# Kernel tuning notes

Hardware: AMD Instinct MI355X
Metric: run time of the kernel (lower is better)

Reference implementation:

```python
import jax, jax.numpy as jnp
import numpy as np

TAU = 2.0        # leak time constant
CLAMP = 1000.0   # state clamp in LeakyRNN.recurrence
EPS = 1e-4       # eps in PolicyRNN.evaluate

B, T, H, NI, NA = 64, 2048, 256, 4, 2


def setup_inputs() -> dict:
    key = jax.random.key(0)
    ks = jax.random.split(key, 10)
    state = jax.random.normal(ks[0], (B, T, NI), jnp.float32)
    last_action = jax.random.normal(ks[1], (B, T, NA), jnp.float32)
    reward = jax.random.randint(ks[2], (B, T, NA), 0, 2).astype(jnp.float32)
    hidden_in = jnp.zeros((B, H), jnp.float32)
    W1 = jax.random.normal(ks[3], (H, NI + 2 * NA), jnp.float32) * np.float32(np.sqrt(2.0 / (NI + 2 * NA)))
    b1 = jnp.zeros((H,), jnp.float32)
    Wih = jax.random.normal(ks[4], (H, H), jnp.float32) * np.float32(np.sqrt(2.0 / H))
    Whh_raw = jax.random.normal(ks[5], (H, H), jnp.float32) * np.float32(0.5 / np.sqrt(H))
    W2 = jax.random.normal(ks[6], (H, H), jnp.float32) * np.float32(np.sqrt(2.0 / H))
    b2 = jnp.zeros((H,), jnp.float32)
    W3 = jax.random.normal(ks[7], (NA, H), jnp.float32) * np.float32(np.sqrt(2.0 / H))
    b3 = jnp.zeros((NA,), jnp.float32)
    Qs = jax.random.normal(ks[8], (B, T, NA), jnp.float32)
    # MultLayerAdaptiveSimple with alphas=[1,0]: weight1=[1,0], weight2=[0,1]
    mix_w = jnp.array([[1.0, 0.0], [0.0, 1.0]], jnp.float32)
    return dict(state=state, last_action=last_action, reward=reward,
                hidden_in=hidden_in, W1=W1, b1=b1, Wih=Wih, Whh_raw=Whh_raw,
                W2=W2, b2=b2, W3=W3, b3=b3, Qs=Qs, mix_w=mix_w)


def reference(state, last_action, reward, hidden_in, W1, b1, Wih, Whh_raw,
              W2, b2, W3, b3, Qs, mix_w):
    # (B,T,.) -> (T,B,.) time-major, matching permute(1,0,2)
    x = jnp.concatenate([reward, state, last_action], -1).transpose(1, 0, 2)
    x = jax.nn.relu(x @ W1.T + b1)                     # linear1 + relu

    # IdentityDiagonal parametrization: zero diagonal, subtract I/tau
    Whh = Whh_raw - jnp.diag(jnp.diag(Whh_raw)) - jnp.eye(H, dtype=Whh_raw.dtype) / TAU
    u = x @ Wih.T                                      # precompute input drive (T,B,H)
    leak = 1.0 - 1.0 / TAU

    def step(h, ut):
        h_new = jnp.clip(leak * h + ut + jax.nn.relu(h) @ Whh.T, -CLAMP, CLAMP)
        return h_new, h_new

    hidden_out, ys = jax.lax.scan(step, hidden_in, u)  # ys: (T,B,H)

    y = jax.nn.relu(ys @ W2.T + b2) @ W3.T + b3        # linear2+relu, linear3
    probs = y.transpose(1, 0, 2)                       # (B,T,NA)

    # evaluate() deterministic path with reward-indexed adaptive mixing
    z = (probs == 0.0).astype(probs.dtype) * EPS
    logp = jnp.log(jax.nn.softmax(probs, -1) + z)
    logq = jnp.log(jax.nn.softmax(Qs, -1) + z)
    # SumOne parametrization (p=1) on each MultLayer 2-vector
    w = jnp.clip(mix_w, -1.0, 1.0)
    table = w / jnp.sum(jnp.abs(w), axis=1, keepdims=True)   # (2,2)
    sel = table[reward[:, :, 0].astype(jnp.int32)]           # (B,T,2)
    mixed = logp * sel[..., :1] + logq * sel[..., 1:2]
    return jnp.exp(mixed), hidden_out
```

## Files before the change

### kernel.cpp

```cpp
#include <hip/hip_runtime.h>
#include <hip/hip_bf16.h>
#include <math.h>

#define Bn 64
#define Tn 2048
#define Hn 256

constexpr float LEAK    = 0.5f;
constexpr float NEGDIAG = -0.5f;
constexpr float CLAMP_V = 1000.0f;
constexpr float EPS_V   = 1e-4f;

typedef __attribute__((ext_vector_type(8))) short  short8;
typedef __attribute__((ext_vector_type(4))) float  f32x4;

#define FAST_BARRIER() do {                                   \
    asm volatile("s_waitcnt lgkmcnt(0)" ::: "memory");        \
    __builtin_amdgcn_s_barrier();                             \
    asm volatile("" ::: "memory");                            \
  } while (0)

__device__ inline short bf16_rne(float x) {
  __hip_bfloat16 h = __float2bfloat16(x);
  return *reinterpret_cast<short*>(&h);
}
__device__ inline float bf16_to_f(short s) {
  union { unsigned u; float f; } c; c.u = ((unsigned)(unsigned short)s) << 16;
  return c.f;
}
__device__ inline unsigned pack2(short a, short b) {
  return (unsigned)(unsigned short)a | ((unsigned)(unsigned short)b << 16);
}

#define SA 40

__global__ __launch_bounds__(512) void g_u(
    const float* __restrict__ reward, const float* __restrict__ state,
    const float* __restrict__ last_action, const float* __restrict__ W1,
    const float* __restrict__ b1, const float* __restrict__ Wih,
    float* __restrict__ u)
{
  __shared__ short Ah[128*SA], Al[128*SA], Bh[256*SA], Bl[256*SA];
  __shared__ __align__(16) float inp_s[128][8];
  __shared__ __align__(16) float w1_s[256][8];
  __shared__ float b1_s[256];
  const int tid = threadIdx.x;
  const int r0  = blockIdx.x * 128;

  for (int idx = tid; idx < 2048; idx += 512) ((float*)w1_s)[idx] = W1[idx];
  if (tid < 256) b1_s[tid] = b1[tid];
  for (int idx = tid; idx < 1024; idx += 512) {
    int rr = idx >> 3, i = idx & 7;
    int r = r0 + rr, b = r & 63, t = r >> 6;
    long base = (long)b * Tn + t;
    float v;
    if (i < 2)      v = reward[base * 2 + i];
    else if (i < 6) v = state[base * 4 + (i - 2)];
    else            v = last_action[base * 2 + (i - 6)];
    inp_s[rr][i] = v;
  }

  const int w    = tid >> 6, lane = tid & 63;
  const int wm   = w >> 2, wn = w & 3;
  const int fr   = lane & 15, fk = lane >> 4;
  f32x4 acc[4][4];
  #pragma unroll
  for (int a = 0; a < 4; ++a)
    #pragma unroll
    for (int c = 0; c < 4; ++c) acc[a][c] = (f32x4){0.f, 0.f, 0.f, 0.f};

  __syncthreads();

  for (int ks = 0; ks < 8; ++ks) {
    const int k0 = ks * 32;
    if (ks) __syncthreads();
    for (int p = tid; p < 2048; p += 512) {
      int rr = p >> 4, kp = (p & 15) * 2;
      int k = k0 + kp;
      float4 iv0 = *reinterpret_cast<const float4*>(&inp_s[rr][0]);
      float4 iv1 = *reinterpret_cast<const float4*>(&inp_s[rr][4]);
      float4 wa0 = *reinterpret_cast<const float4*>(&w1_s[k][0]);
      float4 wa1 = *reinterpret_cast<const float4*>(&w1_s[k][4]);
      float4 wb0 = *reinterpret_cast<const float4*>(&w1_s[k+1][0]);
      float4 wb1 = *reinterpret_cast<const float4*>(&w1_s[k+1][4]);
      float s0 = b1_s[k], s1 = b1_s[k+1];
      s0 = fmaf(iv0.x, wa0.x, s0); s0 = fmaf(iv0.y, wa0.y, s0);
      s0 = fmaf(iv0.z, wa0.z, s0); s0 = fmaf(iv0.w, wa0.w, s0);
      s0 = fmaf(iv1.x, wa1.x, s0); s0 = fmaf(iv1.y, wa1.y, s0);
      s0 = fmaf(iv1.z, wa1.z, s0); s0 = fmaf(iv1.w, wa1.w, s0);
      s1 = fmaf(iv0.x, wb0.x, s1); s1 = fmaf(iv0.y, wb0.y, s1);
      s1 = fmaf(iv0.z, wb0.z, s1); s1 = fmaf(iv0.w, wb0.w, s1);
      s1 = fmaf(iv1.x, wb1.x, s1); s1 = fmaf(iv1.y, wb1.y, s1);
      s1 = fmaf(iv1.z, wb1.z, s1); s1 = fmaf(iv1.w, wb1.w, s1);
      float v0 = fmaxf(s0, 0.f), v1 = fmaxf(s1, 0.f);
      short h0 = bf16_rne(v0), h1 = bf16_rne(v1);
      short l0 = bf16_rne(v0 - bf16_to_f(h0)), l1 = bf16_rne(v1 - bf16_to_f(h1));
      int off = rr * SA + kp;
      *reinterpret_cast<unsigned*>(&Ah[off]) = pack2(h0, h1);
      *reinterpret_cast<unsigned*>(&Al[off]) = pack2(l0, l1);
    }
    for (int c = tid; c < 2048; c += 512) {
      int n = c >> 3, kc = (c & 7) * 4;
      float4 f = *reinterpret_cast<const float4*>(&Wih[n * 256 + k0 + kc]);
      short h0 = bf16_rne(f.x), h1 = bf16_rne(f.y), h2 = bf16_rne(f.z), h3 = bf16_rne(f.w);
      short l0 = bf16_rne(f.x - bf16_to_f(h0)), l1 = bf16_rne(f.y - bf16_to_f(h1));
      short l2 = bf16_rne(f.z - bf16_to_f(h2)), l3 = bf16_rne(f.w - bf16_to_f(h3));
      int off = n * SA + kc;
      *reinterpret_cast<uint2*>(&Bh[off]) = make_uint2(pack2(h0, h1), pack2(h2, h3));
      *reinterpret_cast<uint2*>(&Bl[off]) = make_uint2(pack2(l0, l1), pack2(l2, l3));
    }
    __syncthreads();
    short8 bhf[4], blf[4];
    #pragma unroll
    for (int nf = 0; nf < 4; ++nf) {
      const int brow = wn * 64 + nf * 16 + fr;
      bhf[nf] = *reinterpret_cast<const short8*>(&Bh[brow * SA + fk * 8]);
      blf[nf] = *reinterpret_cast<const short8*>(&Bl[brow * SA + fk * 8]);
    }
    #pragma unroll
    for (int mf = 0; mf < 4; ++mf) {
      const int arow = wm * 64 + mf * 16 + fr;
      short8 ah = *reinterpret_cast<const short8*>(&Ah[arow * SA + fk * 8]);
      short8 al = *reinterpret_cast<const short8*>(&Al[arow * SA + fk * 8]);
      #pragma unroll
      for (int nf = 0; nf < 4; ++nf) {
        acc[mf][nf] = __builtin_amdgcn_mfma_f32_16x16x32_bf16(ah, bhf[nf], acc[mf][nf], 0, 0, 0);
        acc[mf][nf] = __builtin_amdgcn_mfma_f32_16x16x32_bf16(ah, blf[nf], acc[mf][nf], 0, 0, 0);
        acc[mf][nf] = __builtin_amdgcn_mfma_f32_16x16x32_bf16(al, bhf[nf], acc[mf][nf], 0, 0, 0);
      }
    }
  }
  #pragma unroll
  for (int mf = 0; mf < 4; ++mf) {
    const int rbase = r0 + wm * 64 + mf * 16 + (lane >> 4) * 4;
    #pragma unroll
    for (int nf = 0; nf < 4; ++nf) {
      const int n = wn * 64 + nf * 16 + fr;
      #pragma unroll
      for (int j = 0; j < 4; ++j)
        u[(long)(rbase + j) * Hn + n] = acc[mf][nf][j];
    }
  }
}

__global__ __launch_bounds__(1024, 4) void k_scan(
    const float* __restrict__ Whh_raw, const float* __restrict__ hidden_in,
    float* __restrict__ ubuf, float* __restrict__ out)
{
  __shared__ __align__(16) float rh[2][256];
  const int tid = threadIdx.x;
  const int w = tid >> 6;
  const int l = tid & 63;
  const int g = l & 15;
  const int o = l >> 4;
  const int b = blockIdx.x;
  const int kbase = g << 4;

  float wgt[4][16];
  #pragma unroll
  for (int m = 0; m < 4; ++m) {
    const int j = (w << 4) + (o << 2) + m;
    #pragma unroll
    for (int i = 0; i < 16; ++i) {
      const int k = kbase + i;
      float v = Whh_raw[j * 256 + k];
      wgt[m][i] = (k == j) ? NEGDIAG : v;
    }
  }

  const int b0 = g & 1, b1 = (g >> 1) & 1;
  const bool owner = (g < 4);
  const int m_own = (b0 << 1) | b1;
  const int j_own = (w << 4) + (o << 2) + m_own;

  const int wr_off = (j_own & ~15) | ((((j_own >> 2) + (j_own >> 5)) & 3) << 2)
                   | (j_own & 3);

  float h = 0.f, u_cur = 0.f;
  if (owner) {
    h     = hidden_in[b * Hn + j_own];
    u_cur = ubuf[b * Hn + j_own];
  }
  const float* u_ptr  = ubuf + ((long)Bn + b) * Hn + j_own;
  float*       ys_ptr = ubuf + (long)b * Hn + j_own;

  #pragma unroll 2
  for (int t = 0; t < Tn; ++t) {
    const int p = t & 1;
    if (owner) rh[p][wr_off] = fmaxf(h, 0.f);
    FAST_BARRIER();

    float u_nxt = 0.f;
    if (owner && t < Tn - 1) u_nxt = *u_ptr;

    float v0 = 0.f, v1 = 0.f, v2 = 0.f, v3 = 0.f;
    const float* base = &rh[p][kbase];
    #pragma unroll
    for (int q = 0; q < 4; ++q) {
      const int rot = ((((g >> 1) + q) & 3) << 2);
      const float4 r4 = *reinterpret_cast<const float4*>(base + rot);
      v0 = fmaf(r4.x, wgt[0][4*q+0], v0);
      v0 = fmaf(r4.y, wgt[0][4*q+1], v0);
      v0 = fmaf(r4.z, wgt[0][4*q+2], v0);
      v0 = fmaf(r4.w, wgt[0][4*q+3], v0);
      v1 = fmaf(r4.x, wgt[1][4*q+0], v1);
      v1 = fmaf(r4.y, wgt[1][4*q+1], v1);
      v1 = fmaf(r4.z, wgt[1][4*q+2], v1);
      v1 = fmaf(r4.w, wgt[1][4*q+3], v1);
      v2 = fmaf(r4.x, wgt[2][4*q+0], v2);
      v2 = fmaf(r4.y, wgt[2][4*q+1], v2);
      v2 = fmaf(r4.z, wgt[2][4*q+2], v2);
      v2 = fmaf(r4.w, wgt[2][4*q+3], v2);
      v3 = fmaf(r4.x, wgt[3][4*q+0], v3);
      v3 = fmaf(r4.y, wgt[3][4*q+1], v3);
      v3 = fmaf(r4.z, wgt[3][4*q+2], v3);
      v3 = fmaf(r4.w, wgt[3][4*q+3], v3);
    }

    const float s00 = b0 ? v0 : v2;
    const float k00 = b0 ? v2 : v0;
    const float s01 = b0 ? v1 : v3;
    const float k01 = b0 ? v3 : v1;
    const float t00 = k00 + __shfl_xor(s00, 1);
    const float t01 = k01 + __shfl_xor(s01, 1);
    const float s1 = b1 ? t00 : t01;
    const float k1 = b1 ? t01 : t00;
    float s = k1 + __shfl_xor(s1, 2);
    s += __shfl_xor(s, 4);
    s += __shfl_xor(s, 8);

    if (owner) {
      float hn = fmaf(LEAK, h, u_cur) + s;
      hn = fminf(fmaxf(hn, -CLAMP_V), CLAMP_V);
      *ys_ptr = hn;
      h = hn; u_cur = u_nxt;
    }
    ys_ptr += Bn * Hn;
    u_ptr  += Bn * Hn;
  }
  if (owner) out[(long)Bn * Tn * 2 + b * Hn + j_own] = h;
}

__global__ __launch_bounds__(512) void g_out(
    const float* __restrict__ ys, const float* __restrict__ W2,
    const float* __restrict__ b2, const float* __restrict__ W3,
    float* __restrict__ yout)
{
  __shared__ short Ah[128*SA], Al[128*SA], Bh[256*SA], Bl[256*SA];
  __shared__ float b2_s[256];
  __shared__ float w3_s[512];
  const int tid = threadIdx.x;
  const int r0  = blockIdx.x * 128;

  if (tid < 256) b2_s[tid] = b2[tid];
  if (tid < 512) w3_s[tid] = W3[tid];

  const int w    = tid >> 6, lane = tid & 63;
  const int wm   = w >> 2, wn = w & 3;
  const int fr   = lane & 15, fk = lane >> 4;
  f32x4 acc[4][4];
  #pragma unroll
  for (int a = 0; a < 4; ++a)
    #pragma unroll
    for (int c = 0; c < 4; ++c) acc[a][c] = (f32x4){0.f, 0.f, 0.f, 0.f};

  __syncthreads();

  for (int ks = 0; ks < 8; ++ks) {
    const int k0 = ks * 32;
    if (ks) __syncthreads();
    for (int c = tid; c < 1024; c += 512) {
      int rr = c >> 3, kc = (c & 7) * 4;
      float4 f = *reinterpret_cast<const float4*>(&ys[(long)(r0 + rr) * Hn + k0 + kc]);
      short h0 = bf16_rne(f.x), h1 = bf16_rne(f.y), h2 = bf16_rne(f.z), h3 = bf16_rne(f.w);
      short l0 = bf16_rne(f.x - bf16_to_f(h0)), l1 = bf16_rne(f.y - bf16_to_f(h1));
      short l2 = bf16_rne(f.z - bf16_to_f(h2)), l3 = bf16_rne(f.w - bf16_to_f(h3));
      int off = rr * SA + kc;
      *reinterpret_cast<uint2*>(&Ah[off]) = make_uint2(pack2(h0, h1), pack2(h2, h3));
      *reinterpret_cast<uint2*>(&Al[off]) = make_uint2(pack2(l0, l1), pack2(l2, l3));
    }
    for (int c = tid; c < 2048; c += 512) {
      int n = c >> 3, kc = (c & 7) * 4;
      float4 f = *reinterpret_cast<const float4*>(&W2[n * 256 + k0 + kc]);
      short h0 = bf16_rne(f.x), h1 = bf16_rne(f.y), h2 = bf16_rne(f.z), h3 = bf16_rne(f.w);
      short l0 = bf16_rne(f.x - bf16_to_f(h0)), l1 = bf16_rne(f.y - bf16_to_f(h1));
      short l2 = bf16_rne(f.z - bf16_to_f(h2)), l3 = bf16_rne(f.w - bf16_to_f(h3));
      int off = n * SA + kc;
      *reinterpret_cast<uint2*>(&Bh[off]) = make_uint2(pack2(h0, h1), pack2(h2, h3));
      *reinterpret_cast<uint2*>(&Bl[off]) = make_uint2(pack2(l0, l1), pack2(l2, l3));
    }
    __syncthreads();
    short8 bhf[4], blf[4];
    #pragma unroll
    for (int nf = 0; nf < 4; ++nf) {
      const int brow = wn * 64 + nf * 16 + fr;
      bhf[nf] = *reinterpret_cast<const short8*>(&Bh[brow * SA + fk * 8]);
      blf[nf] = *reinterpret_cast<const short8*>(&Bl[brow * SA + fk * 8]);
    }
    #pragma unroll
    for (int mf = 0; mf < 4; ++mf) {
      const int arow = wm * 64 + mf * 16 + fr;
      short8 ah = *reinterpret_cast<const short8*>(&Ah[arow * SA + fk * 8]);
      short8 al = *reinterpret_cast<const short8*>(&Al[arow * SA + fk * 8]);
      #pragma unroll
      for (int nf = 0; nf < 4; ++nf) {
        acc[mf][nf] = __builtin_amdgcn_mfma_f32_16x16x32_bf16(ah, bhf[nf], acc[mf][nf], 0, 0, 0);
        acc[mf][nf] = __builtin_amdgcn_mfma_f32_16x16x32_bf16(ah, blf[nf], acc[mf][nf], 0, 0, 0);
        acc[mf][nf] = __builtin_amdgcn_mfma_f32_16x16x32_bf16(al, bhf[nf], acc[mf][nf], 0, 0, 0);
      }
    }
  }

  float yp[4][4][2];
  #pragma unroll
  for (int mf = 0; mf < 4; ++mf)
    #pragma unroll
    for (int j = 0; j < 4; ++j) { yp[mf][j][0] = 0.f; yp[mf][j][1] = 0.f; }

  #pragma unroll
  for (int mf = 0; mf < 4; ++mf)
    #pragma unroll
    for (int nf = 0; nf < 4; ++nf) {
      const int n = wn * 64 + nf * 16 + fr;
      const float b2v = b2_s[n];
      const float w30 = w3_s[n], w31 = w3_s[256 + n];
      #pragma unroll
      for (int j = 0; j < 4; ++j) {
        float v = fmaxf(acc[mf][nf][j] + b2v, 0.f);
        yp[mf][j][0] = fmaf(v, w30, yp[mf][j][0]);
        yp[mf][j][1] = fmaf(v, w31, yp[mf][j][1]);
      }
    }
  #pragma unroll
  for (int off = 1; off < 16; off <<= 1) {
    #pragma unroll
    for (int mf = 0; mf < 4; ++mf)
      #pragma unroll
      for (int j = 0; j < 4; ++j) {
        yp[mf][j][0] += __shfl_xor(yp[mf][j][0], off);
        yp[mf][j][1] += __shfl_xor(yp[mf][j][1], off);
      }
  }

  __syncthreads();
  float* yred = reinterpret_cast<float*>(Ah);
  if (fr == 0) {
    #pragma unroll
    for (int mf = 0; mf < 4; ++mf)
      #pragma unroll
      for (int j = 0; j < 4; ++j) {
        int rl = wm * 64 + mf * 16 + (lane >> 4) * 4 + j;
        yred[(rl * 2 + 0) * 4 + wn] = yp[mf][j][0];
        yred[(rl * 2 + 1) * 4 + wn] = yp[mf][j][1];
      }
  }
  __syncthreads();
  if (tid < 256) {
    int rl = tid >> 1, a = tid & 1;
    const float* yr = &yred[(rl * 2 + a) * 4];
    float y = (yr[0] + yr[1]) + (yr[2] + yr[3]);
    int r = r0 + rl, b = r & 63, t = r >> 6;
    yout[((long)b * Tn + t) * 2 + a] = y;
  }
}

__global__ __launch_bounds__(256) void k_head(
    float* __restrict__ out, const float* __restrict__ Qs,
    const float* __restrict__ reward, const float* __restrict__ mix_w,
    const float* __restrict__ b3)
{
  const int idx = blockIdx.x * 256 + threadIdx.x;
  if (idx >= Bn * Tn) return;
  const long base = (long)idx * 2;
  float y0 = out[base]     + b3[0];
  float y1 = out[base + 1] + b3[1];
  float z0 = (y0 == 0.f) ? EPS_V : 0.f;
  float z1 = (y1 == 0.f) ? EPS_V : 0.f;

  float m  = fmaxf(y0, y1);
  float e0 = expf(y0 - m), e1 = expf(y1 - m), es = e0 + e1;
  float sp0 = e0 / es, sp1 = e1 / es;

  float q0 = Qs[base], q1 = Qs[base + 1];
  float mq = fmaxf(q0, q1);
  float f0 = expf(q0 - mq), f1 = expf(q1 - mq), fs = f0 + f1;
  float sq0 = f0 / fs, sq1 = f1 / fs;

  int ri = (int)reward[base];
  float m0 = fminf(fmaxf(mix_w[ri * 2 + 0], -1.f), 1.f);
  float m1 = fminf(fmaxf(mix_w[ri * 2 + 1], -1.f), 1.f);
  float den = fabsf(m0) + fabsf(m1);
  float s0 = m0 / den, s1 = m1 / den;

  out[base]     = expf(s0 * logf(sp0 + z0) + s1 * logf(sq0 + z0));
  out[base + 1] = expf(s0 * logf(sp1 + z1) + s1 * logf(sq1 + z1));
}

extern "C" void kernel_launch(void* const* d_in, const int* in_sizes, int n_in,
                              void* d_out, int out_size, void* d_ws, size_t ws_size,
                              hipStream_t stream)
{
  const float* state       = (const float*)d_in[0];
  const float* last_action = (const float*)d_in[1];
  const float* reward      = (const float*)d_in[2];
  const float* hidden_in   = (const float*)d_in[3];
  const float* W1          = (const float*)d_in[4];
  const float* b1          = (const float*)d_in[5];
  const float* Wih         = (const float*)d_in[6];
  const float* Whh_raw     = (const float*)d_in[7];
  const float* W2          = (const float*)d_in[8];
  const float* b2          = (const float*)d_in[9];
  const float* W3          = (const float*)d_in[10];
  const float* b3          = (const float*)d_in[11];
  const float* Qs          = (const float*)d_in[12];
  const float* mix_w       = (const float*)d_in[13];
  float* out = (float*)d_out;
  float* u   = (float*)d_ws;

  const int nrows = Tn * Bn;
  g_u   <<<nrows / 128, 512, 0, stream>>>(reward, state, last_action, W1, b1, Wih, u);
  k_scan<<<Bn,          1024, 0, stream>>>(Whh_raw, hidden_in, u, out);
  g_out <<<nrows / 128, 512, 0, stream>>>(u, W2, b2, W3, out);
  k_head<<<nrows / 256, 256, 0, stream>>>(out, Qs, reward, mix_w, b3);
}
```

Measured before the change: 1.700 ms.

## Run recurrent scan matvec on MFMA with split-bf16 weights and state

The per-timestep Whh·relu(h) product moves from scalar FP32 FMAs plus shuffle reductions over a 1024-thread block to bf16 MFMA instructions in a 256-thread block. Weights and relu(h) are each split into hi and lo bf16 parts, and three MFMAs recover near-FP32 accuracy. The h vector is broadcast across all 16 B columns, so most of each MFMA's work is redundant. The aim is to shorten the serial per-step latency and use a cheaper barrier over fewer waves. The cost is slightly lower precision than true FP32 and heavy register use for the split weights.

```diff
diff --git a/kernel.cpp b/kernel.cpp
--- a/kernel.cpp
+++ b/kernel.cpp
@@ -143,102 +143,133 @@
   }
 }
 
-__global__ __launch_bounds__(1024, 4) void k_scan(
+__global__ __launch_bounds__(256) void k_scan(
     const float* __restrict__ Whh_raw, const float* __restrict__ hidden_in,
     float* __restrict__ ubuf, float* __restrict__ out)
 {
-  __shared__ __align__(16) float rh[2][256];
-  const int tid = threadIdx.x;
-  const int w = tid >> 6;
-  const int l = tid & 63;
-  const int g = l & 15;
-  const int o = l >> 4;
-  const int b = blockIdx.x;
-  const int kbase = g << 4;
-
-  float wgt[4][16];
-  #pragma unroll
-  for (int m = 0; m < 4; ++m) {
-    const int j = (w << 4) + (o << 2) + m;
-    #pragma unroll
-    for (int i = 0; i < 16; ++i) {
-      const int k = kbase + i;
-      float v = Whh_raw[j * 256 + k];
-      wgt[m][i] = (k == j) ? NEGDIAG : v;
-    }
-  }
-
-  const int b0 = g & 1, b1 = (g >> 1) & 1;
-  const bool owner = (g < 4);
-  const int m_own = (b0 << 1) | b1;
-  const int j_own = (w << 4) + (o << 2) + m_own;
-
-  const int wr_off = (j_own & ~15) | ((((j_own >> 2) + (j_own >> 5)) & 3) << 2)
-                   | (j_own & 3);
-
-  float h = 0.f, u_cur = 0.f;
+  __shared__ __align__(16) short rh_s[2][2][256];
+  const int tid  = threadIdx.x;
+  const int w    = tid >> 6;
+  const int lane = tid & 63;
+  const int fr   = lane & 15;
+  const int fk   = lane >> 4;
+  const int b    = blockIdx.x;
+  const bool owner = (fr == 0);
+
+  short8 whi[4][8], wlo[4][8];
+  #pragma unroll
+  for (int mt = 0; mt < 4; ++mt) {
+    const int j = (w * 4 + mt) * 16 + fr;
+    #pragma unroll
+    for (int kt = 0; kt < 8; ++kt) {
+      const int kb = kt * 32 + fk * 8;
+      float4 f0 = *reinterpret_cast<const float4*>(&Whh_raw[j * 256 + kb]);
+      float4 f1 = *reinterpret_cast<const float4*>(&Whh_raw[j * 256 + kb + 4]);
+      float v[8] = {f0.x, f0.y, f0.z, f0.w, f1.x, f1.y, f1.z, f1.w};
+      #pragma unroll
+      for (int e = 0; e < 8; ++e) {
+        if (kb + e == j) v[e] = NEGDIAG;
+        short h = bf16_rne(v[e]);
+        whi[mt][kt][e] = h;
+        wlo[mt][kt][e] = bf16_rne(v[e] - bf16_to_f(h));
+      }
+    }
+  }
+
+  const int fq = lane >> 4;
+  const int jb = w * 64 + fq * 4;
+  float4 h4[4], u4[4];
   if (owner) {
-    h     = hidden_in[b * Hn + j_own];
-    u_cur = ubuf[b * Hn + j_own];
-  }
-  const float* u_ptr  = ubuf + ((long)Bn + b) * Hn + j_own;
-  float*       ys_ptr = ubuf + (long)b * Hn + j_own;
+    #pragma unroll
+    for (int mt = 0; mt < 4; ++mt) {
+      h4[mt] = *reinterpret_cast<const float4*>(&hidden_in[b * Hn + jb + mt * 16]);
+      u4[mt] = *reinterpret_cast<const float4*>(&ubuf[(long)b * Hn + jb + mt * 16]);
+    }
+    #pragma unroll
+    for (int mt = 0; mt < 4; ++mt) {
+      const int j0 = jb + mt * 16;
+      short hh[4], ll[4];
+      #pragma unroll
+      for (int e = 0; e < 4; ++e) {
+        float rv = fmaxf(h4[mt][e], 0.f);
+        hh[e] = bf16_rne(rv);
+        ll[e] = bf16_rne(rv - bf16_to_f(hh[e]));
+      }
+      *reinterpret_cast<uint2*>(&rh_s[0][0][j0]) = make_uint2(pack2(hh[0], hh[1]), pack2(hh[2], hh[3]));
+      *reinterpret_cast<uint2*>(&rh_s[0][1][j0]) = make_uint2(pack2(ll[0], ll[1]), pack2(ll[2], ll[3]));
+    }
+  }
+  __syncthreads();
+
+  const float* u_ptr  = ubuf + ((long)Bn + b) * Hn + jb;
+  float*       ys_ptr = ubuf + (long)b * Hn + jb;
 
   #pragma unroll 2
   for (int t = 0; t < Tn; ++t) {
     const int p = t & 1;
-    if (owner) rh[p][wr_off] = fmaxf(h, 0.f);
+    short8 bh[8], bl[8];
+    #pragma unroll
+    for (int kt = 0; kt < 8; ++kt) {
+      bh[kt] = *reinterpret_cast<const short8*>(&rh_s[p][0][kt * 32 + fk * 8]);
+      bl[kt] = *reinterpret_cast<const short8*>(&rh_s[p][1][kt * 32 + fk * 8]);
+    }
+    float4 un[4];
+    if (owner && t < Tn - 1) {
+      #pragma unroll
+      for (int mt = 0; mt < 4; ++mt)
+        un[mt] = *reinterpret_cast<const float4*>(u_ptr + mt * 16);
+    }
+
+    f32x4 a1[4], a2[4], a3[4];
+    #pragma unroll
+    for (int mt = 0; mt < 4; ++mt) {
+      a1[mt] = (f32x4){0.f, 0.f, 0.f, 0.f};
+      a2[mt] = (f32x4){0.f, 0.f, 0.f, 0.f};
+      a3[mt] = (f32x4){0.f, 0.f, 0.f, 0.f};
+    }
+    #pragma unroll
+    for (int kt = 0; kt < 8; ++kt)
+      #pragma unroll
+      for (int mt = 0; mt < 4; ++mt) {
+        a1[mt] = __builtin_amdgcn_mfma_f32_16x16x32_bf16(whi[mt][kt], bh[kt], a1[mt], 0, 0, 0);
+        a2[mt] = __builtin_amdgcn_mfma_f32_16x16x32_bf16(whi[mt][kt], bl[kt], a2[mt], 0, 0, 0);
+        a3[mt] = __builtin_amdgcn_mfma_f32_16x16x32_bf16(wlo[mt][kt], bh[kt], a3[mt], 0, 0, 0);
+      }
+
+    if (owner) {
+      const int p2 = p ^ 1;
+      #pragma unroll
+      for (int mt = 0; mt < 4; ++mt) {
+        const int j0 = jb + mt * 16;
+        float4 hn;
+        short hh[4], ll[4];
+        #pragma unroll
+        for (int e = 0; e < 4; ++e) {
+          float s = (a1[mt][e] + a2[mt][e]) + a3[mt][e];
+          float v = fmaf(LEAK, h4[mt][e], u4[mt][e]) + s;
+          v = fminf(fmaxf(v, -CLAMP_V), CLAMP_V);
+          hn[e] = v;
+          float rv = fmaxf(v, 0.f);
+          hh[e] = bf16_rne(rv);
+          ll[e] = bf16_rne(rv - bf16_to_f(hh[e]));
+        }
+        *reinterpret_cast<float4*>(ys_ptr + mt * 16) = hn;
+        *reinterpret_cast<uint2*>(&rh_s[p2][0][j0]) = make_uint2(pack2(hh[0], hh[1]), pack2(hh[2], hh[3]));
+        *reinterpret_cast<uint2*>(&rh_s[p2][1][j0]) = make_uint2(pack2(ll[0], ll[1]), pack2(ll[2], ll[3]));
+        h4[mt] = hn;
+        u4[mt] = un[mt];
+      }
+    }
     FAST_BARRIER();
-
-    float u_nxt = 0.f;
-    if (owner && t < Tn - 1) u_nxt = *u_ptr;
-
-    float v0 = 0.f, v1 = 0.f, v2 = 0.f, v3 = 0.f;
-    const float* base = &rh[p][kbase];
-    #pragma unroll
-    for (int q = 0; q < 4; ++q) {
-      const int rot = ((((g >> 1) + q) & 3) << 2);
-      const float4 r4 = *reinterpret_cast<const float4*>(base + rot);
-      v0 = fmaf(r4.x, wgt[0][4*q+0], v0);
-      v0 = fmaf(r4.y, wgt[0][4*q+1], v0);
-      v0 = fmaf(r4.z, wgt[0][4*q+2], v0);
-      v0 = fmaf(r4.w, wgt[0][4*q+3], v0);
-      v1 = fmaf(r4.x, wgt[1][4*q+0], v1);
-      v1 = fmaf(r4.y, wgt[1][4*q+1], v1);
-      v1 = fmaf(r4.z, wgt[1][4*q+2], v1);
-      v1 = fmaf(r4.w, wgt[1][4*q+3], v1);
-      v2 = fmaf(r4.x, wgt[2][4*q+0], v2);
-      v2 = fmaf(r4.y, wgt[2][4*q+1], v2);
-      v2 = fmaf(r4.z, wgt[2][4*q+2], v2);
-      v2 = fmaf(r4.w, wgt[2][4*q+3], v2);
-      v3 = fmaf(r4.x, wgt[3][4*q+0], v3);
-      v3 = fmaf(r4.y, wgt[3][4*q+1], v3);
-      v3 = fmaf(r4.z, wgt[3][4*q+2], v3);
-      v3 = fmaf(r4.w, wgt[3][4*q+3], v3);
-    }
-
-    const float s00 = b0 ? v0 : v2;
-    const float k00 = b0 ? v2 : v0;
-    const float s01 = b0 ? v1 : v3;
-    const float k01 = b0 ? v3 : v1;
-    const float t00 = k00 + __shfl_xor(s00, 1);
-    const float t01 = k01 + __shfl_xor(s01, 1);
-    const float s1 = b1 ? t00 : t01;
-    const float k1 = b1 ? t01 : t00;
-    float s = k1 + __shfl_xor(s1, 2);
-    s += __shfl_xor(s, 4);
-    s += __shfl_xor(s, 8);
-
-    if (owner) {
-      float hn = fmaf(LEAK, h, u_cur) + s;
-      hn = fminf(fmaxf(hn, -CLAMP_V), CLAMP_V);
-      *ys_ptr = hn;
-      h = hn; u_cur = u_nxt;
-    }
     ys_ptr += Bn * Hn;
     u_ptr  += Bn * Hn;
   }
-  if (owner) out[(long)Bn * Tn * 2 + b * Hn + j_own] = h;
+
+  if (owner) {
+    #pragma unroll
+    for (int mt = 0; mt < 4; ++mt)
+      *reinterpret_cast<float4*>(&out[(long)Bn * Tn * 2 + b * Hn + jb + mt * 16]) = h4[mt];
+  }
 }
 
 __global__ __launch_bounds__(512) void g_out(
@@ -419,7 +450,7 @@
 
   const int nrows = Tn * Bn;
   g_u   <<<nrows / 128, 512, 0, stream>>>(reward, state, last_action, W1, b1, Wih, u);
-  k_scan<<<Bn,          1024, 0, stream>>>(Whh_raw, hidden_in, u, out);
+  k_scan<<<Bn,           256, 0, stream>>>(Whh_raw, hidden_in, u, out);
   g_out <<<nrows / 128, 512, 0, stream>>>(u, W2, b2, W3, out);
   k_head<<<nrows / 256, 256, 0, stream>>>(out, Qs, reward, mix_w, b3);
 }
```

Result: slower. 3.099 ms (+82.2%).

## Use packed FMA, ds_swizzle reductions, and deeper u prefetch in recurrent scan

Applied to the files above, without the earlier changes.

The per-step matvec in the sequential scan now uses v_pk_fma_f32 on pairs of weights, which halves the FMA instruction count, and keeps two partial accumulators per output. The cross-lane reductions switch from __shfl_xor (ds_bpermute) to ds_swizzle xor patterns, and the u input is prefetched two steps ahead instead of one. The loop is manually unrolled by two with fixed buffer indices. The packed accumulators change the floating-point summation order slightly, and the inline asm may limit how the compiler schedules the loop.

```diff
diff --git a/kernel.cpp b/kernel.cpp
--- a/kernel.cpp
+++ b/kernel.cpp
@@ -13,6 +13,7 @@
 
 typedef __attribute__((ext_vector_type(8))) short  short8;
 typedef __attribute__((ext_vector_type(4))) float  f32x4;
+typedef __attribute__((ext_vector_type(2))) float  f32x2;
 
 #define FAST_BARRIER() do {                                   \
     asm volatile("s_waitcnt lgkmcnt(0)" ::: "memory");        \
@@ -31,6 +32,10 @@
 __device__ inline unsigned pack2(short a, short b) {
   return (unsigned)(unsigned short)a | ((unsigned)(unsigned short)b << 16);
 }
+__device__ inline void pkfma(f32x2& a, f32x2 x, f32x2 y) {
+  asm("v_pk_fma_f32 %0, %1, %2, %0" : "+v"(a) : "v"(x), "v"(y));
+}
+#define SWZ(x, imm) __int_as_float(__builtin_amdgcn_ds_swizzle(__float_as_int(x), (imm)))
 
 #define SA 40
 
@@ -156,15 +161,18 @@
   const int b = blockIdx.x;
   const int kbase = g << 4;
 
-  float wgt[4][16];
+  f32x2 w2[4][8];
   #pragma unroll
   for (int m = 0; m < 4; ++m) {
     const int j = (w << 4) + (o << 2) + m;
     #pragma unroll
-    for (int i = 0; i < 16; ++i) {
-      const int k = kbase + i;
-      float v = Whh_raw[j * 256 + k];
-      wgt[m][i] = (k == j) ? NEGDIAG : v;
+    for (int i = 0; i < 8; ++i) {
+      const int k = kbase + i * 2;
+      float a = Whh_raw[j * 256 + k];
+      float c = Whh_raw[j * 256 + k + 1];
+      if (k == j)     a = NEGDIAG;
+      if (k + 1 == j) c = NEGDIAG;
+      w2[m][i] = (f32x2){a, c};
     }
   }
 
@@ -175,69 +183,69 @@
 
   const int wr_off = (j_own & ~15) | ((((j_own >> 2) + (j_own >> 5)) & 3) << 2)
                    | (j_own & 3);
-
-  float h = 0.f, u_cur = 0.f;
+  int a_q[4];
+  #pragma unroll
+  for (int q = 0; q < 4; ++q) a_q[q] = kbase + (((((g >> 1) + q) & 3)) << 2);
+
+  float h = 0.f, u_c = 0.f, u_n = 0.f;
   if (owner) {
-    h     = hidden_in[b * Hn + j_own];
-    u_cur = ubuf[b * Hn + j_own];
-  }
-  const float* u_ptr  = ubuf + ((long)Bn + b) * Hn + j_own;
+    h   = hidden_in[b * Hn + j_own];
+    u_c = ubuf[b * Hn + j_own];
+    u_n = ubuf[((long)Bn + b) * Hn + j_own];
+  }
+  const float* u_ptr  = ubuf + ((long)2 * Bn + b) * Hn + j_own;
   float*       ys_ptr = ubuf + (long)b * Hn + j_own;
 
-  #pragma unroll 2
-  for (int t = 0; t < Tn; ++t) {
-    const int p = t & 1;
-    if (owner) rh[p][wr_off] = fmaxf(h, 0.f);
-    FAST_BARRIER();
-
-    float u_nxt = 0.f;
-    if (owner && t < Tn - 1) u_nxt = *u_ptr;
-
-    float v0 = 0.f, v1 = 0.f, v2 = 0.f, v3 = 0.f;
-    const float* base = &rh[p][kbase];
-    #pragma unroll
-    for (int q = 0; q < 4; ++q) {
-      const int rot = ((((g >> 1) + q) & 3) << 2);
-      const float4 r4 = *reinterpret_cast<const float4*>(base + rot);
-      v0 = fmaf(r4.x, wgt[0][4*q+0], v0);
-      v0 = fmaf(r4.y, wgt[0][4*q+1], v0);
-      v0 = fmaf(r4.z, wgt[0][4*q+2], v0);
-      v0 = fmaf(r4.w, wgt[0][4*q+3], v0);
-      v1 = fmaf(r4.x, wgt[1][4*q+0], v1);
-      v1 = fmaf(r4.y, wgt[1][4*q+1], v1);
-      v1 = fmaf(r4.z, wgt[1][4*q+2], v1);
-      v1 = fmaf(r4.w, wgt[1][4*q+3], v1);
-      v2 = fmaf(r4.x, wgt[2][4*q+0], v2);
-      v2 = fmaf(r4.y, wgt[2][4*q+1], v2);
-      v2 = fmaf(r4.z, wgt[2][4*q+2], v2);
-      v2 = fmaf(r4.w, wgt[2][4*q+3], v2);
-      v3 = fmaf(r4.x, wgt[3][4*q+0], v3);
-      v3 = fmaf(r4.y, wgt[3][4*q+1], v3);
-      v3 = fmaf(r4.z, wgt[3][4*q+2], v3);
-      v3 = fmaf(r4.w, wgt[3][4*q+3], v3);
-    }
-
-    const float s00 = b0 ? v0 : v2;
-    const float k00 = b0 ? v2 : v0;
-    const float s01 = b0 ? v1 : v3;
-    const float k01 = b0 ? v3 : v1;
-    const float t00 = k00 + __shfl_xor(s00, 1);
-    const float t01 = k01 + __shfl_xor(s01, 1);
-    const float s1 = b1 ? t00 : t01;
-    const float k1 = b1 ? t01 : t00;
-    float s = k1 + __shfl_xor(s1, 2);
-    s += __shfl_xor(s, 4);
-    s += __shfl_xor(s, 8);
-
-    if (owner) {
-      float hn = fmaf(LEAK, h, u_cur) + s;
-      hn = fminf(fmaxf(hn, -CLAMP_V), CLAMP_V);
-      *ys_ptr = hn;
-      h = hn; u_cur = u_nxt;
-    }
-    ys_ptr += Bn * Hn;
-    u_ptr  += Bn * Hn;
-  }
+#define SCAN_STEP(P)                                                         \
+  {                                                                          \
+    if (owner) rh[P][wr_off] = fmaxf(h, 0.f);                                \
+    FAST_BARRIER();                                                          \
+    float u_pf = 0.f;                                                        \
+    if (owner && t + 2 < Tn) u_pf = *u_ptr;                                  \
+    float4 r[4];                                                             \
+    r[0] = *reinterpret_cast<const float4*>(&rh[P][a_q[0]]);                 \
+    r[1] = *reinterpret_cast<const float4*>(&rh[P][a_q[1]]);                 \
+    r[2] = *reinterpret_cast<const float4*>(&rh[P][a_q[2]]);                 \
+    r[3] = *reinterpret_cast<const float4*>(&rh[P][a_q[3]]);                 \
+    f32x2 c0 = {0.f, 0.f}, c1 = {0.f, 0.f}, c2 = {0.f, 0.f}, c3 = {0.f, 0.f};\
+    _Pragma("unroll")                                                        \
+    for (int q = 0; q < 4; ++q) {                                            \
+      const f32x2 rlo = {r[q].x, r[q].y};                                    \
+      const f32x2 rhi = {r[q].z, r[q].w};                                    \
+      pkfma(c0, rlo, w2[0][2*q]); pkfma(c0, rhi, w2[0][2*q+1]);              \
+      pkfma(c1, rlo, w2[1][2*q]); pkfma(c1, rhi, w2[1][2*q+1]);              \
+      pkfma(c2, rlo, w2[2][2*q]); pkfma(c2, rhi, w2[2][2*q+1]);              \
+      pkfma(c3, rlo, w2[3][2*q]); pkfma(c3, rhi, w2[3][2*q+1]);              \
+    }                                                                        \
+    const float v0 = c0.x + c0.y, v1 = c1.x + c1.y;                          \
+    const float v2 = c2.x + c2.y, v3 = c3.x + c3.y;                          \
+    const float s00 = b0 ? v0 : v2;                                          \
+    const float k00 = b0 ? v2 : v0;                                          \
+    const float s01 = b0 ? v1 : v3;                                          \
+    const float k01 = b0 ? v3 : v1;                                          \
+    const float t00 = k00 + SWZ(s00, 0x041F);                                \
+    const float t01 = k01 + SWZ(s01, 0x041F);                                \
+    const float s1 = b1 ? t00 : t01;                                         \
+    const float k1 = b1 ? t01 : t00;                                         \
+    float s = k1 + SWZ(s1, 0x081F);                                          \
+    s += SWZ(s, 0x101F);                                                     \
+    s += SWZ(s, 0x201F);                                                     \
+    if (owner) {                                                             \
+      float hn = fmaf(LEAK, h, u_c) + s;                                     \
+      hn = fminf(fmaxf(hn, -CLAMP_V), CLAMP_V);                              \
+      *ys_ptr = hn;                                                          \
+      h = hn; u_c = u_n; u_n = u_pf;                                         \
+    }                                                                        \
+    ys_ptr += Bn * Hn;                                                       \
+    u_ptr  += Bn * Hn;                                                       \
+  }
+
+  for (int tt = 0; tt < Tn; tt += 2) {
+    { const int t = tt;     SCAN_STEP(0) }
+    { const int t = tt + 1; SCAN_STEP(1) }
+  }
+#undef SCAN_STEP
+
   if (owner) out[(long)Bn * Tn * 2 + b * Hn + j_own] = h;
 }
 
```

Measured after the change: 1.638 ms. 1.04x faster.
